# Kernel optimization log

Hardware: AMD Instinct MI355X
Metric: run time of the kernel (lower is better)

Reference implementation:

```python
import jax, jax.numpy as jnp
import numpy as np

B, N = 4, 512
C_IN, H, W = 1024, 48, 48
IMG_H, IMG_W = 48.0, 48.0
CNN_EMB, BOX_EMB, GCN_OUT = 512, 256, 512
ROWS, COLS = 58, 30
ALPHA = 5.0
K_EDGES = 8 * N  # edges kept per image per graph

# all directed pairs (i != j) of a fully-connected graph on N nodes
_ii, _jj = np.meshgrid(np.arange(N), np.arange(N), indexing='ij')
_m = _ii != _jj
PAIRS = jnp.asarray(np.stack([_ii[_m], _jj[_m]], axis=1).astype(np.int32))  # [E,2]


def setup_inputs():
    key = jax.random.key(0)
    ks = jax.random.split(key, 12)
    x = jax.random.normal(ks[0], (B, C_IN, H, W), jnp.float32)
    # valid boxes (x1<x2, y1<y2) inside the 48x48 feature map
    p = jax.random.uniform(ks[1], (B, N, 2, 2), minval=0.0, maxval=float(W) - 2.0)
    lo = jnp.min(p, axis=2)
    hi = jnp.max(p, axis=2) + 1.0
    boxes = jnp.concatenate([lo, hi], axis=-1)  # [B,N,4] x1,y1,x2,y2

    def lin(k, fi, fo):
        return jax.random.normal(k, (fi, fo), jnp.float32) / np.sqrt(fi)

    return {
        'input': x, 'boxes': boxes,
        'im_scales': jnp.ones((B,), jnp.float32),
        'pdls': jnp.zeros((B,), jnp.float32),
        'pdts': jnp.zeros((B,), jnp.float32),
        'W_dec': jax.random.normal(ks[2], (256, C_IN, 3, 3), jnp.float32) / np.sqrt(C_IN * 9.0),
        'b_dec': jnp.zeros((256,), jnp.float32),
        'W_box': lin(ks[3], 4, BOX_EMB), 'b_box': jnp.zeros((BOX_EMB,), jnp.float32),
        'W_cnn': lin(ks[4], 256 * 4, CNN_EMB), 'b_cnn': jnp.zeros((CNN_EMB,), jnp.float32),
        'W_grow': lin(ks[5], CNN_EMB + BOX_EMB, GCN_OUT), 'b_grow': jnp.zeros((GCN_OUT,), jnp.float32),
        'W_gcol': lin(ks[6], CNN_EMB + BOX_EMB, GCN_OUT), 'b_gcol': jnp.zeros((GCN_OUT,), jnp.float32),
        'W_rcls': lin(ks[7], GCN_OUT, 2 * (ROWS - 1) * 2), 'b_rcls': jnp.zeros((2 * (ROWS - 1) * 2,), jnp.float32),
        'W_ccls': lin(ks[8], GCN_OUT, 2 * (COLS - 1) * 2), 'b_ccls': jnp.zeros((2 * (COLS - 1) * 2,), jnp.float32),
    }


def _bilinear(feat, bidx, py, px):
    # feat [B,C,H,W]; py,px [M,4] sample coords -> [M,4,C]
    Hh, Ww = feat.shape[2], feat.shape[3]
    py = jnp.clip(py, 0.0, Hh - 1.0)
    px = jnp.clip(px, 0.0, Ww - 1.0)
    y0 = jnp.floor(py).astype(jnp.int32)
    x0 = jnp.floor(px).astype(jnp.int32)
    y1 = jnp.minimum(y0 + 1, Hh - 1)
    x1 = jnp.minimum(x0 + 1, Ww - 1)
    wy = (py - y0)[..., None]
    wx = (px - x0)[..., None]
    b = bidx[:, None]
    f00 = feat[b, :, y0, x0]
    f01 = feat[b, :, y0, x1]
    f10 = feat[b, :, y1, x0]
    f11 = feat[b, :, y1, x1]
    return f00 * (1 - wy) * (1 - wx) + f01 * (1 - wy) * wx + f10 * wy * (1 - wx) + f11 * wy * wx


def _roi_align_2x2(feat, boxes, bidx):
    # roi_align output_size=2, spatial_scale=1, one sample per bin (bin center)
    x1, y1, x2, y2 = boxes[:, 0], boxes[:, 1], boxes[:, 2], boxes[:, 3]
    bw = (x2 - x1) / 2.0
    bh = (y2 - y1) / 2.0
    offs = jnp.array([0.5, 1.5], jnp.float32)
    sx = x1[:, None] + offs * bw[:, None]  # [M,2]
    sy = y1[:, None] + offs * bh[:, None]
    py = sy[:, jnp.array([0, 0, 1, 1])]  # (iy, ix) ordering
    px = sx[:, jnp.array([0, 1, 0, 1])]
    val = _bilinear(feat, bidx, py, px)  # [M,4,C]
    return jnp.transpose(val, (0, 2, 1)).reshape(val.shape[0], -1)  # [M, C*2*2]


def _edge_attrs(boxes_i, scale, pdl, pdt):
    org = (boxes_i - jnp.stack([pdl, pdt, pdl, pdt])) / scale
    cx = (org[:, 0] + org[:, 2]) * 0.5
    cy = (org[:, 1] + org[:, 3]) * 0.5
    tb_w = jnp.max(org[:, jnp.array([0, 2])])
    tb_h = jnp.max(org[:, jnp.array([1, 3])])
    s, d = PAIRS[:, 0], PAIRS[:, 1]
    row_attr = jnp.exp(-jnp.square((cy[s] - cy[d]) * ALPHA / tb_h))
    col_attr = jnp.exp(-jnp.square((cx[s] - cx[d]) * ALPHA / tb_w))
    rv, ri = jax.lax.top_k(row_attr, K_EDGES)
    cv, ci = jax.lax.top_k(col_attr, K_EDGES)
    return rv, PAIRS[ri], cv, PAIRS[ci]


def _gcn(x, Wg, bg, edges, ew, num_nodes):
    # PyG GCNConv: self-loops with weight 1, symmetric normalization
    loop = jnp.arange(num_nodes, dtype=edges.dtype)
    src = jnp.concatenate([edges[0], loop])
    dst = jnp.concatenate([edges[1], loop])
    w = jnp.concatenate([ew, jnp.ones((num_nodes,), ew.dtype)])
    deg = jax.ops.segment_sum(w, dst, num_segments=num_nodes)
    dis = jax.lax.rsqrt(deg)  # deg >= 1 thanks to self-loops
    norm = dis[src] * w * dis[dst]
    xw = x @ Wg
    agg = jax.ops.segment_sum(norm[:, None] * xw[src], dst, num_segments=num_nodes)
    return agg + bg


def _forward(input, boxes, im_scales, pdls, pdts, W_dec, b_dec, W_box, b_box,
             W_cnn, b_cnn, W_grow, b_grow, W_gcol, b_gcol, W_rcls, b_rcls, W_ccls, b_ccls):
    Bn = B * N
    flat = boxes.reshape(Bn, 4)
    # box features (relative center / size)
    cx = (flat[:, 0] + flat[:, 2]) / 2.0
    cy = (flat[:, 1] + flat[:, 3]) / 2.0
    bf = jnp.stack([cx / IMG_W, cy / IMG_H,
                    (flat[:, 2] - flat[:, 0]) / IMG_W,
                    (flat[:, 3] - flat[:, 1]) / IMG_H], axis=1)
    box_feat = jax.nn.relu(bf @ W_box + b_box)
    # decode conv + relu
    dec = jax.lax.conv_general_dilated(input, W_dec, (1, 1), 'SAME',
                                       dimension_numbers=('NCHW', 'OIHW', 'NCHW'))
    dec = jax.nn.relu(dec + b_dec[None, :, None, None])
    # roi-align 2x2 + cnn embedding
    bidx = jnp.repeat(jnp.arange(B, dtype=jnp.int32), N)
    cnn = _roi_align_2x2(dec, flat, bidx)
    cnn_feat = jax.nn.relu(cnn @ W_cnn + b_cnn)
    # per-image dense graph -> top-8N row/col edges
    rv, re, cv, ce = jax.vmap(_edge_attrs)(boxes, im_scales, pdls, pdts)
    off = (jnp.arange(B, dtype=jnp.int32) * N)[:, None, None]
    row_edge = (re + off).reshape(-1, 2).T  # [2, B*K]
    col_edge = (ce + off).reshape(-1, 2).T
    row_w = rv.reshape(-1)
    col_w = cv.reshape(-1)
    fusion = jnp.concatenate([box_feat, cnn_feat], axis=1)  # [Bn, 768]
    row_feat = jax.nn.relu(_gcn(fusion, W_grow, b_grow, row_edge, row_w, Bn))
    col_feat = jax.nn.relu(_gcn(fusion, W_gcol, b_gcol, col_edge, col_w, Bn))
    row_score = jax.nn.leaky_relu(row_feat @ W_rcls + b_rcls, 0.01).reshape(Bn, 2, ROWS - 1, 2)
    col_score = jax.nn.leaky_relu(col_feat @ W_ccls + b_ccls, 0.01).reshape(Bn, 2, COLS - 1, 2)
    return row_score, col_score


def reference(input, boxes, im_scales, pdls, pdts, W_dec, b_dec, W_box, b_box,
              W_cnn, b_cnn, W_grow, b_grow, W_gcol, b_gcol, W_rcls, b_rcls, W_ccls, b_ccls):
    return _forward(input, boxes, im_scales, pdls, pdts, W_dec, b_dec, W_box, b_box,
                    W_cnn, b_cnn, W_grow, b_grow, W_gcol, b_gcol,
                    W_rcls, b_rcls, W_ccls, b_ccls)
```

## Files before the change

### kernel.cpp

```cpp
#include <hip/hip_runtime.h>
#include <cstdint>
#include <math.h>

typedef unsigned int u32;
typedef unsigned long long u64;
typedef unsigned short ushort;

typedef __attribute__((ext_vector_type(8))) _Float16 f16x8;
typedef __attribute__((ext_vector_type(4))) _Float16 f16x4;
typedef __attribute__((ext_vector_type(4))) float f32x4;

#define NB    4
#define BnN   2048
#define NE    261632
#define NCHUNK 16
#define ECHUNK 16352
#define KEDGE 4096
#define TIECAP 2048
#define PSLICE 2359296
#define MS    64
#define TS    64

#define GLD16(gsrc, ldst)                                                    \
    __builtin_amdgcn_global_load_lds(                                        \
        (const __attribute__((address_space(1))) void*)(gsrc),               \
        (__attribute__((address_space(3))) void*)(ldst), 16, 0, 0)

__global__ __launch_bounds__(256) void cvt_x_kernel(
    const float* __restrict__ in, _Float16* __restrict__ xf)
{
    __shared__ _Float16 sh[64][49];
    int cg = blockIdx.x, y = blockIdx.y, b = blockIdx.z;
    int tid = threadIdx.x;
    for (int i = tid; i < 64 * 48; i += 256) {
        int cl = i / 48, x = i - cl * 48;
        sh[cl][x] = (_Float16)in[(((size_t)b * 1024 + cg * 64 + cl) * 48 + y) * 48 + x];
    }
    __syncthreads();
    for (int i = tid; i < 64 * 48; i += 256) {
        int x = i / 64, cl = i - x * 64;
        xf[((size_t)(b * 48 + y) * 48 + x) * 1024 + cg * 64 + cl] = sh[cl][x];
    }
}

__global__ __launch_bounds__(256) void cvt_w_kernel(
    const float* __restrict__ W, _Float16* __restrict__ wf)
{
    __shared__ _Float16 sh[9216];
    int o = blockIdx.x, tid = threadIdx.x;
    for (int g = tid; g < 9216; g += 256)
        sh[g] = (_Float16)W[(size_t)o * 9216 + g];
    __syncthreads();
    for (int g = tid; g < 9216; g += 256) {
        int tap = g >> 10, ch = g & 1023;
        wf[(size_t)o * 9216 + g] = sh[ch * 9 + tap];
    }
}

__global__ __launch_bounds__(256) void cvt_t5_kernel(
    const float* __restrict__ Wc,  _Float16* __restrict__ WcT,
    const float* __restrict__ Wgr, _Float16* __restrict__ WgrT,
    const float* __restrict__ Wgc, _Float16* __restrict__ WgcT,
    const float* __restrict__ Wr,  _Float16* __restrict__ WrT,
    const float* __restrict__ Wcc, _Float16* __restrict__ WccT)
{
    __shared__ _Float16 sh[32][33];
    int bid = blockIdx.x;
    const float* in; _Float16* out; int K, N, tx0, ty0, ntx;
    if (bid < 512)       { in = Wc;  out = WcT;  K = 1024; N = 512; ntx = 16; bid -= 0;    }
    else if (bid < 896)  { in = Wgr; out = WgrT; K = 768;  N = 512; ntx = 16; bid -= 512;  }
    else if (bid < 1280) { in = Wgc; out = WgcT; K = 768;  N = 512; ntx = 16; bid -= 896;  }
    else if (bid < 1408) { in = Wr;  out = WrT;  K = 512;  N = 228; ntx = 8;  bid -= 1280; }
    else                 { in = Wcc; out = WccT; K = 512;  N = 116; ntx = 4;  bid -= 1408; }
    tx0 = (bid % ntx) * 32;
    ty0 = (bid / ntx) * 32;
    int tx = threadIdx.x & 31, ty = threadIdx.x >> 5;
#pragma unroll
    for (int i = 0; i < 4; ++i) {
        int k = ty0 + ty + i * 8, n = tx0 + tx;
        sh[ty + i * 8][tx] = (k < K && n < N) ? (_Float16)in[(size_t)k * N + n] : (_Float16)0.f;
    }
    __syncthreads();
#pragma unroll
    for (int i = 0; i < 4; ++i) {
        int n = tx0 + ty + i * 8, k = ty0 + tx;
        if (n < N && k < K) out[(size_t)n * K + k] = sh[tx][ty + i * 8];
    }
}

#define STAGE(cc)                                                            \
    {                                                                        \
        _Pragma("unroll")                                                    \
        for (int it = 0; it < 5; ++it) {                                     \
            if (it * 256 + wv * 64 < 1152)                                   \
                GLD16(wsrc[it] + (cc), &wS[(it * 256 + wv * 64) * 8]);       \
        }                                                                    \
        _Pragma("unroll")                                                    \
        for (int it = 0; it < 8; ++it)                                       \
            GLD16(xsrc[it] + (cc), &xS[(it * 256 + wv * 64) * 8]);           \
    }

#define LDB(BUF, R)                                                          \
    {                                                                        \
        _Pragma("unroll")                                                    \
        for (int u = 0; u < 9; ++u) {                                        \
            int nt_ = u / 3, dx_ = u % 3;                                    \
            BUF[u] = *(const f16x8*)&xS[(((R) * 4 + q) * 50 + nt_ * 16 + n + dx_) * 8]; \
        }                                                                    \
    }

#define DOTAP(TAP, BLO, BHI)                                                 \
    {                                                                        \
        _Pragma("unroll")                                                    \
        for (int dx_ = 0; dx_ < 3; ++dx_) {                                  \
            f16x8 a0 = *(const f16x8*)&wS[(((TAP) + dx_) * 128 + q * 32 + n) * 8];      \
            f16x8 a1 = *(const f16x8*)&wS[(((TAP) + dx_) * 128 + q * 32 + 16 + n) * 8]; \
            _Pragma("unroll")                                                \
            for (int nt_ = 0; nt_ < 3; ++nt_) {                              \
                f16x8 blo = BLO[nt_ * 3 + dx_];                              \
                f16x8 bhi = BHI[nt_ * 3 + dx_];                              \
                acc[0][0][nt_] = __builtin_amdgcn_mfma_f32_16x16x32_f16(a0, blo, acc[0][0][nt_], 0, 0, 0); \
                acc[1][0][nt_] = __builtin_amdgcn_mfma_f32_16x16x32_f16(a1, blo, acc[1][0][nt_], 0, 0, 0); \
                acc[0][1][nt_] = __builtin_amdgcn_mfma_f32_16x16x32_f16(a0, bhi, acc[0][1][nt_], 0, 0, 0); \
                acc[1][1][nt_] = __builtin_amdgcn_mfma_f32_16x16x32_f16(a1, bhi, acc[1][1][nt_], 0, 0, 0); \
            }                                                                \
        }                                                                    \
    }

__global__ __launch_bounds__(256, 3) void conv_part_kernel(
    const _Float16* __restrict__ xf, const _Float16* __restrict__ wf,
    const _Float16* __restrict__ zbuf, float* __restrict__ pbuf)
{
    __shared__ _Float16 wS[1152 * 8];
    __shared__ _Float16 xS[2048 * 8];
    const int p = blockIdx.x;
    const int L = (p & 7) * 96 + (p >> 3);
    const int og = L & 7;
    const int t  = L >> 3;
    const int xt = t % 6;
    const int bz = t / 6;
    const int y0 = xt * 8;
    const int b  = bz >> 2, ks = bz & 3;
    const int tid = threadIdx.x;
    const int wv = tid >> 6;
    const int ln = tid & 63;
    const int n  = ln & 15;
    const int q  = ln >> 4;

    f32x4 acc[2][2][3];
#pragma unroll
    for (int mt = 0; mt < 2; ++mt)
#pragma unroll
        for (int rr = 0; rr < 2; ++rr)
#pragma unroll
            for (int nt = 0; nt < 3; ++nt) acc[mt][rr][nt] = (f32x4){0.f, 0.f, 0.f, 0.f};

    const _Float16* wsrc[5];
    const _Float16* xsrc[8];
#pragma unroll
    for (int it = 0; it < 5; ++it) {
        int g = it * 256 + tid;
        int gg = (g < 1152) ? g : 0;
        int tap = gg >> 7, r = gg & 127, qq = r >> 5, oc = r & 31;
        wsrc[it] = wf + (size_t)(((og * 32 + oc) * 9 + tap) * 1024 + qq * 8);
    }
#pragma unroll
    for (int it = 0; it < 8; ++it) {
        int g = it * 256 + tid;
        int row = g / 200, r2 = g - row * 200;
        int qq = r2 / 50, c = r2 - qq * 50;
        int gy = y0 + row - 1, gx = c - 1;
        bool inb = (g < 2000) && ((unsigned)gy < 48u) && ((unsigned)gx < 48u);
        xsrc[it] = inb ? (xf + (size_t)(((b * 48 + gy) * 48 + gx) * 1024 + qq * 8)) : zbuf;
    }

    const int c0 = ks * 256;
    const int rbase = 2 * wv;

    STAGE(c0);

#pragma unroll 1
    for (int ci = 0; ci < 8; ++ci) {
        asm volatile("s_waitcnt vmcnt(0)" ::: "memory");
        __syncthreads();

        __builtin_amdgcn_s_setprio(1);
        f16x8 bA[9], bB[9];
        LDB(bA, rbase + 0);
        LDB(bB, rbase + 1);
        DOTAP(0, bA, bB);
        LDB(bA, rbase + 2);
        DOTAP(3, bB, bA);
        LDB(bB, rbase + 3);
        DOTAP(6, bA, bB);
        __builtin_amdgcn_s_setprio(0);
        __syncthreads();
        if (ci < 7) STAGE(c0 + (ci + 1) * 32);
    }

#pragma unroll
    for (int rr = 0; rr < 2; ++rr) {
        const int y = y0 + 2 * wv + rr;
#pragma unroll
        for (int mt = 0; mt < 2; ++mt) {
#pragma unroll
            for (int nt = 0; nt < 3; ++nt) {
                int x = nt * 16 + n;
                *(f32x4*)(pbuf + (size_t)ks * PSLICE +
                          ((size_t)(b * 48 + y) * 48 + x) * 256 + og * 32 + mt * 16 + q * 4) = acc[mt][rr][nt];
            }
        }
    }
}

__global__ __launch_bounds__(256) void conv_sum_kernel(
    const float* __restrict__ pbuf, const float* __restrict__ bd,
    _Float16* __restrict__ dec)
{
    size_t idx = (size_t)blockIdx.x * 256 + threadIdx.x;
    size_t e = idx * 4;
    int och = (int)(e & 255);
    f32x4 s0 = *(const f32x4*)(pbuf + e);
    f32x4 s1 = *(const f32x4*)(pbuf + (size_t)PSLICE + e);
    f32x4 s2 = *(const f32x4*)(pbuf + (size_t)2 * PSLICE + e);
    f32x4 s3 = *(const f32x4*)(pbuf + (size_t)3 * PSLICE + e);
    float4 b4 = *(const float4*)(bd + och);
    f16x4 v;
    v.x = (_Float16)fmaxf(s0[0] + s1[0] + s2[0] + s3[0] + b4.x, 0.f);
    v.y = (_Float16)fmaxf(s0[1] + s1[1] + s2[1] + s3[1] + b4.y, 0.f);
    v.z = (_Float16)fmaxf(s0[2] + s1[2] + s2[2] + s3[2] + b4.z, 0.f);
    v.w = (_Float16)fmaxf(s0[3] + s1[3] + s2[3] + s3[3] + b4.w, 0.f);
    *(f16x4*)(dec + e) = v;
}

__global__ __launch_bounds__(256) void roi_box_kernel(
    const _Float16* __restrict__ dec, const float* __restrict__ boxes,
    const float* __restrict__ Wb, const float* __restrict__ bb,
    _Float16* __restrict__ cnn, _Float16* __restrict__ fusion)
{
    int n = blockIdx.x; int c = threadIdx.x;
    int b = n >> 9;
    float x1 = boxes[n * 4 + 0], y1 = boxes[n * 4 + 1];
    float x2 = boxes[n * 4 + 2], y2 = boxes[n * 4 + 3];
    {
        float bf0 = ((x1 + x2) * 0.5f) / 48.f;
        float bf1 = ((y1 + y2) * 0.5f) / 48.f;
        float bf2 = (x2 - x1) / 48.f;
        float bf3 = (y2 - y1) / 48.f;
        float acc = bb[c];
        acc += bf0 * Wb[0 * 256 + c];
        acc += bf1 * Wb[1 * 256 + c];
        acc += bf2 * Wb[2 * 256 + c];
        acc += bf3 * Wb[3 * 256 + c];
        fusion[(size_t)n * 768 + c] = (_Float16)fmaxf(acc, 0.f);
    }
    float bw = (x2 - x1) * 0.5f, bh = (y2 - y1) * 0.5f;
    float sxv[2] = { x1 + 0.5f * bw, x1 + 1.5f * bw };
    float syv[2] = { y1 + 0.5f * bh, y1 + 1.5f * bh };
    float px[4] = { sxv[0], sxv[1], sxv[0], sxv[1] };
    float py[4] = { syv[0], syv[0], syv[1], syv[1] };
    const _Float16* f = dec + (size_t)b * 2304 * 256;
    f16x4 o4;
    float res[4];
#pragma unroll
    for (int p = 0; p < 4; ++p) {
        float yy = fminf(fmaxf(py[p], 0.f), 47.f);
        float xx = fminf(fmaxf(px[p], 0.f), 47.f);
        int y0 = (int)floorf(yy), x0 = (int)floorf(xx);
        int y1i = min(y0 + 1, 47), x1i = min(x0 + 1, 47);
        float wy = yy - (float)y0, wx = xx - (float)x0;
        float f00 = (float)f[(size_t)(y0 * 48 + x0) * 256 + c];
        float f01 = (float)f[(size_t)(y0 * 48 + x1i) * 256 + c];
        float f10 = (float)f[(size_t)(y1i * 48 + x0) * 256 + c];
        float f11 = (float)f[(size_t)(y1i * 48 + x1i) * 256 + c];
        res[p] = f00 * (1.f - wy) * (1.f - wx) + f01 * (1.f - wy) * wx
               + f10 * wy * (1.f - wx) + f11 * wy * wx;
    }
    o4.x = (_Float16)res[0]; o4.y = (_Float16)res[1];
    o4.z = (_Float16)res[2]; o4.w = (_Float16)res[3];
    *(f16x4*)(cnn + (size_t)n * 1024 + c * 4) = o4;
}

#define GEMM_STAGE(cc, bi)                                                   \
    {                                                                        \
        GLD16(asrc + (cc), &aS[bi][(wv * 64) * 8]);                          \
        GLD16(bsrc + (cc), &bS[bi][(wv * 64) * 8]);                          \
    }

template <int ACT, typename OUTT>
__global__ __launch_bounds__(256) void gemm16_kernel(
    const _Float16* __restrict__ A, const _Float16* __restrict__ Bt,
    const _Float16* __restrict__ zbuf,
    const float* __restrict__ bias, OUTT* __restrict__ C,
    int M, int N, int K, int ldC)
{
    __shared__ _Float16 aS[2][256 * 8];
    __shared__ _Float16 bS[2][256 * 8];
    const int n0 = blockIdx.x * 64, m0 = blockIdx.y * 64;
    const int tid = threadIdx.x;
    const int wv = tid >> 6, ln = tid & 63;
    const int wm = wv & 1, wn = wv >> 1;
    const int lm = ln & 15, lq = ln >> 4;
    const int sr = tid >> 2, sq = tid & 3;

    const _Float16* asrc = A + (size_t)(m0 + sr) * K + sq * 8;
    const _Float16* bsrc = (n0 + sr < N) ? (Bt + (size_t)(n0 + sr) * K + sq * 8) : zbuf;

    f32x4 acc[2][2];
#pragma unroll
    for (int i = 0; i < 2; ++i)
#pragma unroll
        for (int j = 0; j < 2; ++j) acc[i][j] = (f32x4){0.f, 0.f, 0.f, 0.f};

    const int NT = K >> 5;
    GEMM_STAGE(0, 0);
#pragma unroll 1
    for (int it = 0; it < NT; ++it) {
        const int bi = it & 1;
        if (it + 1 < NT) {
            GEMM_STAGE((it + 1) * 32, bi ^ 1);
            asm volatile("s_waitcnt vmcnt(2)" ::: "memory");
        } else {
            asm volatile("s_waitcnt vmcnt(0)" ::: "memory");
        }
        __builtin_amdgcn_s_barrier();
        f16x8 af[2], bf[2];
#pragma unroll
        for (int mt = 0; mt < 2; ++mt) af[mt] = *(const f16x8*)&aS[bi][(wm * 32 + mt * 16 + lm) * 32 + lq * 8];
#pragma unroll
        for (int nt = 0; nt < 2; ++nt) bf[nt] = *(const f16x8*)&bS[bi][(wn * 32 + nt * 16 + lm) * 32 + lq * 8];
#pragma unroll
        for (int mt = 0; mt < 2; ++mt)
#pragma unroll
            for (int nt = 0; nt < 2; ++nt)
                acc[mt][nt] = __builtin_amdgcn_mfma_f32_16x16x32_f16(af[mt], bf[nt], acc[mt][nt], 0, 0, 0);
        __builtin_amdgcn_sched_barrier(0);
        __builtin_amdgcn_s_barrier();
    }

#pragma unroll
    for (int mt = 0; mt < 2; ++mt) {
#pragma unroll
        for (int nt = 0; nt < 2; ++nt) {
            int col = n0 + wn * 32 + nt * 16 + lm;
            if (col >= N) continue;
            float bs = bias ? bias[col] : 0.f;
#pragma unroll
            for (int r = 0; r < 4; ++r) {
                int row = m0 + wm * 32 + mt * 16 + lq * 4 + r;
                float v = acc[mt][nt][r] + bs;
                if (ACT == 1) v = fmaxf(v, 0.f);
                if (ACT == 2) v = (v >= 0.f) ? v : 0.01f * v;
                C[(size_t)row * ldC + col] = (OUTT)v;
            }
        }
    }
}

__global__ __launch_bounds__(256) void gemm16z_kernel(
    const _Float16* __restrict__ A,
    const _Float16* __restrict__ Bt0, const _Float16* __restrict__ Bt1,
    const _Float16* __restrict__ zbuf,
    float* __restrict__ C0, float* __restrict__ C1,
    int M, int N, int K, int ldC)
{
    const _Float16* __restrict__ Bt = blockIdx.z ? Bt1 : Bt0;
    float* __restrict__ C = blockIdx.z ? C1 : C0;
    __shared__ _Float16 aS[2][256 * 8];
    __shared__ _Float16 bS[2][256 * 8];
    const int n0 = blockIdx.x * 64, m0 = blockIdx.y * 64;
    const int tid = threadIdx.x;
    const int wv = tid >> 6, ln = tid & 63;
    const int wm = wv & 1, wn = wv >> 1;
    const int lm = ln & 15, lq = ln >> 4;
    const int sr = tid >> 2, sq = tid & 3;

    const _Float16* asrc = A + (size_t)(m0 + sr) * K + sq * 8;
    const _Float16* bsrc = (n0 + sr < N) ? (Bt + (size_t)(n0 + sr) * K + sq * 8) : zbuf;

    f32x4 acc[2][2];
#pragma unroll
    for (int i = 0; i < 2; ++i)
#pragma unroll
        for (int j = 0; j < 2; ++j) acc[i][j] = (f32x4){0.f, 0.f, 0.f, 0.f};

    const int NT = K >> 5;
    GEMM_STAGE(0, 0);
#pragma unroll 1
    for (int it = 0; it < NT; ++it) {
        const int bi = it & 1;
        if (it + 1 < NT) {
            GEMM_STAGE((it + 1) * 32, bi ^ 1);
            asm volatile("s_waitcnt vmcnt(2)" ::: "memory");
        } else {
            asm volatile("s_waitcnt vmcnt(0)" ::: "memory");
        }
        __builtin_amdgcn_s_barrier();
        f16x8 af[2], bf[2];
#pragma unroll
        for (int mt = 0; mt < 2; ++mt) af[mt] = *(const f16x8*)&aS[bi][(wm * 32 + mt * 16 + lm) * 32 + lq * 8];
#pragma unroll
        for (int nt = 0; nt < 2; ++nt) bf[nt] = *(const f16x8*)&bS[bi][(wn * 32 + nt * 16 + lm) * 32 + lq * 8];
#pragma unroll
        for (int mt = 0; mt < 2; ++mt)
#pragma unroll
            for (int nt = 0; nt < 2; ++nt)
                acc[mt][nt] = __builtin_amdgcn_mfma_f32_16x16x32_f16(af[mt], bf[nt], acc[mt][nt], 0, 0, 0);
        __builtin_amdgcn_sched_barrier(0);
        __builtin_amdgcn_s_barrier();
    }

#pragma unroll
    for (int mt = 0; mt < 2; ++mt) {
#pragma unroll
        for (int nt = 0; nt < 2; ++nt) {
            int col = n0 + wn * 32 + nt * 16 + lm;
            if (col >= N) continue;
#pragma unroll
            for (int r = 0; r < 4; ++r) {
                int row = m0 + wm * 32 + mt * 16 + lq * 4 + r;
                C[(size_t)row * ldC + col] = acc[mt][nt][r];
            }
        }
    }
}

__device__ __forceinline__ float compute_sv_tb(
    const float* __restrict__ boxes, const float* __restrict__ scales,
    const float* __restrict__ pdls, const float* __restrict__ pdts,
    int b, int t, float* sv, float* red)
{
    int tid = threadIdx.x;
    float pdl = pdls[b], pdt = pdts[b], sc = scales[b];
    if (tid < 512) {
        const float* bx = boxes + (size_t)(b * 512 + tid) * 4;
        float o0 = (bx[0] - pdl) / sc;
        float o1 = (bx[1] - pdt) / sc;
        float o2 = (bx[2] - pdl) / sc;
        float o3 = (bx[3] - pdt) / sc;
        sv[tid]  = (t == 0) ? (o1 + o3) * 0.5f : (o0 + o2) * 0.5f;
        red[tid] = (t == 0) ? fmaxf(o1, o3)    : fmaxf(o0, o2);
    }
    __syncthreads();
    for (int s = 256; s > 0; s >>= 1) {
        if (tid < s) red[tid] = fmaxf(red[tid], red[tid + s]);
        __syncthreads();
    }
    float tbv = red[0];
    __syncthreads();
    return tbv;
}

#define QBITS(e, QB)                                                   \
    {                                                                  \
        int i_ = (e) / 511; int jj_ = (e) - i_ * 511;                  \
        int j_ = jj_ + (jj_ >= i_ ? 1 : 0);                            \
        float diff_ = sv[i_] - sv[j_];                                 \
        float u_ = (diff_ * 5.0f) / tbv;                               \
        float q_ = u_ * u_;                                            \
        QB = __float_as_uint(q_);                                      \
    }

__global__ __launch_bounds__(1024) void histA_kernel(
    const float* __restrict__ boxes, const float* __restrict__ scales,
    const float* __restrict__ pdls, const float* __restrict__ pdts,
    u32* __restrict__ gpart)
{
    __shared__ float sv[512]; __shared__ float red[512];
    __shared__ u32 lh[4096];
    const int sel = blockIdx.y, b = sel >> 1, t = sel & 1;
    const int tid = threadIdx.x;
    for (int i = tid; i < 4096; i += 1024) lh[i] = 0;
    const float tbv = compute_sv_tb(boxes, scales, pdls, pdts, b, t, sv, red);
    const int e1 = min((int)(blockIdx.x + 1) * ECHUNK, NE);
    for (int e = blockIdx.x * ECHUNK + tid; e < e1; e += 1024) {
        u32 qb; QBITS(e, qb);
        atomicAdd(&lh[qb >> 20], 1u);
    }
    __syncthreads();
    u32* G = gpart + ((size_t)sel * NCHUNK + blockIdx.x) * 4096;
    for (int i = tid; i < 4096; i += 1024) G[i] = lh[i];
}

__global__ __launch_bounds__(1024) void scanA_kernel(
    const u32* __restrict__ gpart, u32* __restrict__ meta)
{
    const int sel = blockIdx.x, tid = threadIdx.x;
    __shared__ u32 bins[4096];
    __shared__ u32 sc[2][1024];
    for (int b = tid; b < 4096; b += 1024) {
        u32 s = 0;
        for (int c = 0; c < NCHUNK; ++c) s += gpart[((size_t)sel * NCHUNK + c) * 4096 + b];
        bins[b] = s;
    }
    __syncthreads();
    u32 part = 0;
#pragma unroll
    for (int j = 0; j < 4; ++j) part += bins[tid * 4 + j];
    sc[0][tid] = part;
    __syncthreads();
    int src = 0;
    for (int st = 1; st < 1024; st <<= 1) {
        sc[1 - src][tid] = sc[src][tid] + (tid >= st ? sc[src][tid - st] : 0);
        __syncthreads(); src = 1 - src;
    }
    u32 inc = sc[src][tid], exc = inc - part;
    if (exc < (u32)KEDGE && (u32)KEDGE <= inc) {
        u32 cum = exc;
        for (int j = 0; j < 4; ++j) {
            u32 c = bins[tid * 4 + j];
            if (cum + c >= (u32)KEDGE) {
                meta[sel * MS + 0] = (u32)(tid * 4 + j);
                meta[sel * MS + 1] = (u32)KEDGE - cum;
                break;
            }
            cum += c;
        }
    }
}

__global__ __launch_bounds__(1024) void histB_kernel(
    const float* __restrict__ boxes, const float* __restrict__ scales,
    const float* __restrict__ pdls, const float* __restrict__ pdts,
    const u32* __restrict__ meta, u32* __restrict__ gpart)
{
    __shared__ float sv[512]; __shared__ float red[512];
    __shared__ u32 lh[4096];
    const int sel = blockIdx.y, b = sel >> 1, t = sel & 1;
    const int tid = threadIdx.x;
    for (int i = tid; i < 4096; i += 1024) lh[i] = 0;
    const float tbv = compute_sv_tb(boxes, scales, pdls, pdts, b, t, sv, red);
    const u32 p12 = meta[sel * MS + 0];
    const int e1 = min((int)(blockIdx.x + 1) * ECHUNK, NE);
    for (int e = blockIdx.x * ECHUNK + tid; e < e1; e += 1024) {
        u32 qb; QBITS(e, qb);
        if ((qb >> 20) == p12) atomicAdd(&lh[(qb >> 8) & 0xFFF], 1u);
    }
    __syncthreads();
    u32* G = gpart + ((size_t)sel * NCHUNK + blockIdx.x) * 4096;
    for (int i = tid; i < 4096; i += 1024) G[i] = lh[i];
}

__global__ __launch_bounds__(1024) void scanB_kernel(
    const u32* __restrict__ gpart, u32* __restrict__ meta)
{
    const int sel = blockIdx.x, tid = threadIdx.x;
    const u32 TH = meta[sel * MS + 1];
    __shared__ u32 bins[4096];
    __shared__ u32 sc[2][1024];
    for (int b = tid; b < 4096; b += 1024) {
        u32 s = 0;
        for (int c = 0; c < NCHUNK; ++c) s += gpart[((size_t)sel * NCHUNK + c) * 4096 + b];
        bins[b] = s;
    }
    __syncthreads();
    u32 part = 0;
#pragma unroll
    for (int j = 0; j < 4; ++j) part += bins[tid * 4 + j];
    sc[0][tid] = part;
    __syncthreads();
    int src = 0;
    for (int st = 1; st < 1024; st <<= 1) {
        sc[1 - src][tid] = sc[src][tid] + (tid >= st ? sc[src][tid - st] : 0);
        __syncthreads(); src = 1 - src;
    }
    u32 inc = sc[src][tid], exc = inc - part;
    if (exc < TH && TH <= inc) {
        u32 cum = exc;
        for (int j = 0; j < 4; ++j) {
            u32 c = bins[tid * 4 + j];
            if (cum + c >= TH) {
                meta[sel * MS + 6] = (meta[sel * MS + 0] << 12) | (u32)(tid * 4 + j);
                meta[sel * MS + 7] = TH - cum;
                break;
            }
            cum += c;
        }
    }
}

__global__ __launch_bounds__(1024) void histC_kernel(
    const float* __restrict__ boxes, const float* __restrict__ scales,
    const float* __restrict__ pdls, const float* __restrict__ pdts,
    const u32* __restrict__ meta, u32* __restrict__ gpart)
{
    __shared__ float sv[512]; __shared__ float red[512];
    __shared__ u32 lh[256];
    const int sel = blockIdx.y, b = sel >> 1, t = sel & 1;
    const int tid = threadIdx.x;
    if (tid < 256) lh[tid] = 0;
    const float tbv = compute_sv_tb(boxes, scales, pdls, pdts, b, t, sv, red);
    const u32 p24 = meta[sel * MS + 6];
    const int e1 = min((int)(blockIdx.x + 1) * ECHUNK, NE);
    for (int e = blockIdx.x * ECHUNK + tid; e < e1; e += 1024) {
        u32 qb; QBITS(e, qb);
        if ((qb >> 8) == p24) atomicAdd(&lh[qb & 0xFF], 1u);
    }
    __syncthreads();
    u32* G = gpart + ((size_t)sel * NCHUNK + blockIdx.x) * 256;
    if (tid < 256) G[tid] = lh[tid];
}

__global__ __launch_bounds__(256) void scanC_kernel(
    const u32* __restrict__ gpart, u32* __restrict__ meta)
{
    const int sel = blockIdx.x, tid = threadIdx.x;
    const u32 TH = meta[sel * MS + 7];
    __shared__ u32 bins[256];
    __shared__ u32 sc[2][256];
    __shared__ u32 s_qstar;
    u32 s = 0;
    for (int c = 0; c < NCHUNK; ++c) s += gpart[((size_t)sel * NCHUNK + c) * 256 + tid];
    bins[tid] = s;
    sc[0][tid] = s;
    __syncthreads();
    int src = 0;
    for (int st = 1; st < 256; st <<= 1) {
        sc[1 - src][tid] = sc[src][tid] + (tid >= st ? sc[src][tid - st] : 0);
        __syncthreads(); src = 1 - src;
    }
    u32 inc = sc[src][tid], exc = inc - bins[tid];
    if (exc < TH && TH <= inc)
        s_qstar = (meta[sel * MS + 6] << 8) | (u32)tid;
    __syncthreads();
    if (tid == 0) {
        u32 prefix = s_qstar;
        float qstar = __uint_as_float(prefix);
        float wstar = (float)exp(-(double)qstar);
        u32 lo = 0, hi = prefix;
        while (lo < hi) {
            u32 mid = (lo + hi) >> 1;
            float wm = (float)exp(-(double)__uint_as_float(mid));
            if (wm > wstar) lo = mid + 1; else hi = mid;
        }
        meta[sel * MS + 2] = lo;
        lo = prefix; hi = 0x7F800000u;
        while (lo < hi) {
            u32 mid = (lo + hi + 1) >> 1;
            float wm = (float)exp(-(double)__uint_as_float(mid));
            if (wm < wstar) hi = mid - 1; else lo = mid;
        }
        meta[sel * MS + 3] = lo;
        meta[sel * MS + 4] = __float_as_uint(wstar);
    }
}

__global__ __launch_bounds__(1024) void emit_kernel(
    const float* __restrict__ boxes, const float* __restrict__ scales,
    const float* __restrict__ pdls, const float* __restrict__ pdts,
    u32* __restrict__ meta, int* __restrict__ tiebuf, int* __restrict__ tiecnt,
    int* __restrict__ es, int* __restrict__ ed, float* __restrict__ ewt,
    int* __restrict__ indeg, float* __restrict__ degw)
{
    __shared__ float sv[512]; __shared__ float red[512];
    __shared__ int s_wcnt, s_tcnt, s_wbase, s_tbase;
    const int sel = blockIdx.y, b = sel >> 1, t = sel & 1;
    const int tid = threadIdx.x;
    const float tbv = compute_sv_tb(boxes, scales, pdls, pdts, b, t, sv, red);
    const u32 qlo = meta[sel * MS + 2], qhi = meta[sel * MS + 3];
    const int base = t * 16384 + b * 4096;
    const int e0 = blockIdx.x * ECHUNK + tid;
    const int e1 = min((int)(blockIdx.x + 1) * ECHUNK, NE);
    if (tid == 0) { s_wcnt = 0; s_tcnt = 0; }
    __syncthreads();
    int myw = 0, myt = 0;
    for (int e = e0; e < e1; e += 1024) {
        u32 qb; QBITS(e, qb);
        if (qb < qlo) ++myw;
        else if (qb <= qhi) ++myt;
    }
    if (myw) atomicAdd(&s_wcnt, myw);
    if (myt) atomicAdd(&s_tcnt, myt);
    __syncthreads();
    if (tid == 0) {
        s_wbase = (s_wcnt > 0) ? (int)atomicAdd(&meta[sel * MS + 5], (u32)s_wcnt) : 0;
        s_tbase = (s_tcnt > 0) ? atomicAdd(&tiecnt[sel * TS], s_tcnt) : 0;
        s_wcnt = 0; s_tcnt = 0;
    }
    __syncthreads();
    for (int e = e0; e < e1; e += 1024) {
        u32 qb; QBITS(e, qb);
        if (qb < qlo) {
            int i = e / 511; int jj = e - i * 511; int j = jj + (jj >= i ? 1 : 0);
            float wval = (float)exp(-(double)__uint_as_float(qb));
            int slot = s_wbase + atomicAdd(&s_wcnt, 1);
            es[base + slot] = b * 512 + i;
            ed[base + slot] = b * 512 + j;
            ewt[base + slot] = wval;
            atomicAdd(&indeg[t * 2048 + b * 512 + j], 1);
            atomicAdd(&degw[t * 2048 + b * 512 + j], wval);
        } else if (qb <= qhi) {
            int p = s_tbase + atomicAdd(&s_tcnt, 1);
            if (p < TIECAP) tiebuf[sel * TIECAP + p] = e;
        }
    }
}

__global__ __launch_bounds__(1024) void tie_scan_fill_kernel(
    u32* __restrict__ meta, const int* __restrict__ tiebuf, const int* __restrict__ tiecnt,
    int* __restrict__ es, int* __restrict__ ed, float* __restrict__ ewt,
    int* __restrict__ indeg, float* __restrict__ degw,
    int* __restrict__ offs, float* __restrict__ dis, int* __restrict__ csr)
{
    __shared__ int bufA[2048], bufB[2048];
    __shared__ int fill_l[2048];
    const int t = blockIdx.x, tid = threadIdx.x;
    for (int b = 0; b < 4; ++b) {
        int sel = b * 2 + t;
        int m = min(tiecnt[sel * TS], TIECAP);
        int r = KEDGE - (int)meta[sel * MS + 5];
        float wt = __uint_as_float(meta[sel * MS + 4]);
        int base = t * 16384 + b * 4096;
        for (int k = tid; k < m; k += 1024) {
            int e = tiebuf[sel * TIECAP + k];
            int rank = 0;
            for (int l = 0; l < m; ++l) rank += (tiebuf[sel * TIECAP + l] < e) ? 1 : 0;
            if (rank < r) {
                int i = e / 511; int jj = e - i * 511; int j = jj + (jj >= i ? 1 : 0);
                int slot = (int)atomicAdd(&meta[sel * MS + 5], 1u);
                es[base + slot] = b * 512 + i;
                ed[base + slot] = b * 512 + j;
                ewt[base + slot] = wt;
                atomicAdd(&indeg[t * 2048 + b * 512 + j], 1);
                atomicAdd(&degw[t * 2048 + b * 512 + j], wt);
            }
        }
    }
    __threadfence();
    __syncthreads();
    bufA[tid] = indeg[t * 2048 + tid];
    bufA[tid + 1024] = indeg[t * 2048 + tid + 1024];
    fill_l[tid] = 0; fill_l[tid + 1024] = 0;
    __syncthreads();
    int* src = bufA; int* dst = bufB;
    for (int st = 1; st < 2048; st <<= 1) {
        dst[tid] = src[tid] + (tid >= st ? src[tid - st] : 0);
        int k1 = tid + 1024;
        dst[k1] = src[k1] + (k1 >= st ? src[k1 - st] : 0);
        __syncthreads();
        int* tmp = src; src = dst; dst = tmp;
    }
    int off0 = (tid == 0) ? 0 : src[tid - 1];
    int off1 = src[tid + 1023];
    __syncthreads();
    dst[tid] = off0; dst[tid + 1024] = off1;
    offs[t * 2048 + tid] = off0;
    offs[t * 2048 + tid + 1024] = off1;
    dis[t * 2048 + tid] = 1.0f / sqrtf(1.0f + degw[t * 2048 + tid]);
    dis[t * 2048 + tid + 1024] = 1.0f / sqrtf(1.0f + degw[t * 2048 + tid + 1024]);
    __syncthreads();
    for (int e = tid; e < 16384; e += 1024) {
        int dl = ed[t * 16384 + e] & 2047;
        int pos = dst[dl] + atomicAdd(&fill_l[dl], 1);
        csr[t * 16384 + pos] = e;
    }
}

__global__ __launch_bounds__(256) void gcn_agg_kernel(
    const float* __restrict__ xw_row, const float* __restrict__ xw_col,
    const float* __restrict__ b_row, const float* __restrict__ b_col,
    const int* __restrict__ es, const float* __restrict__ ew,
    const int* __restrict__ csr, const int* __restrict__ offs,
    const int* __restrict__ indeg, const float* __restrict__ dis,
    _Float16* __restrict__ feat_row, _Float16* __restrict__ feat_col)
{
    int d = blockIdx.x; int t = blockIdx.y;
    const float* xw = t ? xw_col : xw_row;
    const float* bg = t ? b_col : b_row;
    _Float16* out = t ? feat_col : feat_row;
    int f0 = threadIdx.x, f1 = threadIdx.x + 256;
    float dd = dis[t * 2048 + d];
    float a0 = dd * dd * xw[(size_t)d * 512 + f0];
    float a1 = dd * dd * xw[(size_t)d * 512 + f1];
    int st = offs[t * 2048 + d], cnt = indeg[t * 2048 + d];
    for (int k = 0; k < cnt; ++k) {
        int e = csr[t * 16384 + st + k];
        int s = es[t * 16384 + e];
        float w = ew[t * 16384 + e];
        float coef = dis[t * 2048 + s] * w * dd;
        a0 += coef * xw[(size_t)s * 512 + f0];
        a1 += coef * xw[(size_t)s * 512 + f1];
    }
    a0 += bg[f0]; a1 += bg[f1];
    out[(size_t)d * 512 + f0] = (_Float16)fmaxf(a0, 0.f);
    out[(size_t)d * 512 + f1] = (_Float16)fmaxf(a1, 0.f);
}

extern "C" void kernel_launch(void* const* d_in, const int* in_sizes, int n_in,
                              void* d_out, int out_size, void* d_ws, size_t ws_size,
                              hipStream_t stream)
{
    const float* x      = (const float*)d_in[0];
    const float* boxes  = (const float*)d_in[1];
    const float* scales = (const float*)d_in[2];
    const float* pdls   = (const float*)d_in[3];
    const float* pdts   = (const float*)d_in[4];
    const float* W_dec  = (const float*)d_in[5];
    const float* b_dec  = (const float*)d_in[6];
    const float* W_box  = (const float*)d_in[7];
    const float* b_box  = (const float*)d_in[8];
    const float* W_cnn  = (const float*)d_in[9];
    const float* b_cnn  = (const float*)d_in[10];
    const float* W_grow = (const float*)d_in[11];
    const float* b_grow = (const float*)d_in[12];
    const float* W_gcol = (const float*)d_in[13];
    const float* b_gcol = (const float*)d_in[14];
    const float* W_rcls = (const float*)d_in[15];
    const float* b_rcls = (const float*)d_in[16];
    const float* W_ccls = (const float*)d_in[17];
    const float* b_ccls = (const float*)d_in[18];

    char* ws = (char*)d_ws;
    size_t off = 0;
    auto alloc = [&](size_t bytes) -> void* {
        void* p = ws + off;
        off = (off + bytes + 255) & ~(size_t)255;
        return p;
    };
    _Float16* xf16   = (_Float16*)alloc((size_t)4 * 2304 * 1024 * 2);
    _Float16* wf16   = (_Float16*)alloc((size_t)256 * 9216 * 2);
    _Float16* dec    = (_Float16*)alloc((size_t)4 * 2304 * 256 * 2);
    float*    pbuf   = (float*)   alloc((size_t)4 * PSLICE * 4);
    _Float16* cnn    = (_Float16*)alloc((size_t)2048 * 1024 * 2);
    _Float16* fusion = (_Float16*)alloc((size_t)2048 * 768 * 2);
    _Float16* WcT    = (_Float16*)alloc((size_t)512 * 1024 * 2);
    _Float16* WgrT   = (_Float16*)alloc((size_t)512 * 768 * 2);
    _Float16* WgcT   = (_Float16*)alloc((size_t)512 * 768 * 2);
    _Float16* WrT    = (_Float16*)alloc((size_t)228 * 512 * 2);
    _Float16* WccT   = (_Float16*)alloc((size_t)116 * 512 * 2);
    float* xw        = (float*)alloc((size_t)2097152 * 4);
    _Float16* feats  = (_Float16*)alloc((size_t)2 * 2048 * 512 * 2);
    int*  es     = (int*)  alloc((size_t)2 * 16384 * 4);
    int*  ed     = (int*)  alloc((size_t)2 * 16384 * 4);
    float* ewt   = (float*)alloc((size_t)2 * 16384 * 4);
    int*  offsA  = (int*)  alloc((size_t)4096 * 4);
    float* dis   = (float*)alloc((size_t)4096 * 4);
    int*  csr    = (int*)  alloc((size_t)2 * 16384 * 4);
    int*  tiebuf = (int*)  alloc((size_t)8 * TIECAP * 4);
    u32*  gpartA = (u32*)  alloc((size_t)8 * NCHUNK * 4096 * 4);
    u32*  gpartB = (u32*)  alloc((size_t)8 * NCHUNK * 4096 * 4);
    u32*  gpartC = (u32*)  alloc((size_t)8 * NCHUNK * 256 * 4);
    size_t z0 = off;
    u32*  meta   = (u32*)  alloc((size_t)8 * MS * 4);
    int*  tiecnt = (int*)  alloc((size_t)8 * TS * 4);
    int*  indeg  = (int*)  alloc((size_t)4096 * 4);
    float* degw  = (float*)alloc((size_t)4096 * 4);
    _Float16* zbuf = (_Float16*)alloc((size_t)4096);
    size_t z1 = off;

    float* out = (float*)d_out;

    hipMemsetAsync(ws + z0, 0, z1 - z0, stream);

    cvt_x_kernel<<<dim3(16, 48, 4), 256, 0, stream>>>(x, xf16);
    cvt_w_kernel<<<256, 256, 0, stream>>>(W_dec, wf16);
    conv_part_kernel<<<dim3(768), 256, 0, stream>>>(xf16, wf16, zbuf, pbuf);
    conv_sum_kernel<<<2304, 256, 0, stream>>>(pbuf, b_dec, dec);
    roi_box_kernel<<<2048, 256, 0, stream>>>(dec, boxes, W_box, b_box, cnn, fusion);
    cvt_t5_kernel<<<1472, 256, 0, stream>>>(W_cnn, WcT, W_grow, WgrT, W_gcol, WgcT,
                                            W_rcls, WrT, W_ccls, WccT);
    gemm16_kernel<1, _Float16><<<dim3(8, 32), 256, 0, stream>>>(cnn, WcT, zbuf, b_cnn, fusion + 256, 2048, 512, 1024, 768);
    histA_kernel<<<dim3(NCHUNK, 8), 1024, 0, stream>>>(boxes, scales, pdls, pdts, gpartA);
    scanA_kernel<<<8, 1024, 0, stream>>>(gpartA, meta);
    histB_kernel<<<dim3(NCHUNK, 8), 1024, 0, stream>>>(boxes, scales, pdls, pdts, meta, gpartB);
    scanB_kernel<<<8, 1024, 0, stream>>>(gpartB, meta);
    histC_kernel<<<dim3(NCHUNK, 8), 1024, 0, stream>>>(boxes, scales, pdls, pdts, meta, gpartC);
    scanC_kernel<<<8, 256, 0, stream>>>(gpartC, meta);
    emit_kernel<<<dim3(NCHUNK, 8), 1024, 0, stream>>>(boxes, scales, pdls, pdts, meta,
                                                      tiebuf, tiecnt, es, ed, ewt, indeg, degw);
    tie_scan_fill_kernel<<<2, 1024, 0, stream>>>(meta, tiebuf, tiecnt, es, ed, ewt,
                                                 indeg, degw, offsA, dis, csr);
    gemm16z_kernel<<<dim3(8, 32, 2), 256, 0, stream>>>(fusion, WgrT, WgcT, zbuf, xw, xw + 1048576,
                                                       2048, 512, 768, 512);
    gcn_agg_kernel<<<dim3(2048, 2), 256, 0, stream>>>(xw, xw + 1048576, b_grow, b_gcol,
                                                      es, ewt, csr, offsA, indeg, dis,
                                                      feats, feats + (size_t)2048 * 512);
    gemm16_kernel<2, float><<<dim3(4, 32), 256, 0, stream>>>(feats, WrT, zbuf, b_rcls, out, 2048, 228, 512, 228);
    gemm16_kernel<2, float><<<dim3(2, 32), 256, 0, stream>>>(feats + (size_t)2048 * 512, WccT, zbuf, b_ccls,
                                                             out + (size_t)2048 * 228, 2048, 116, 512, 116);
}
```

Before: 348.2 us.

## Double-buffer conv input tiles and drop horizontal halo from LDS staging

The input activation tile in the conv partial kernel is now double-buffered in LDS, so the next channel chunk's input loads are issued before the current chunk's MFMA work, with partial vmcnt waits. The x-halo columns are no longer staged; edge lanes read from a small zero buffer in LDS instead, which shrinks each tile from 2000 to 1920 vectors. Weight staging stays single-buffered and is issued after the compute barrier. The larger LDS footprint lowers the launch bound from 3 to 2 blocks per CU, trading occupancy for overlap of loads with compute.

New measurement: 353.3 us. No clear change (+1.5%).

```diff
diff --git a/kernel.cpp b/kernel.cpp
--- a/kernel.cpp
+++ b/kernel.cpp
@@ -88,16 +88,24 @@
     }
 }
 
-#define STAGE(cc)                                                            \
+#define STAGE_X(cc, BUF)                                                     \
+    {                                                                        \
+        _Pragma("unroll")                                                    \
+        for (int it = 0; it < 8; ++it) {                                     \
+            int g0 = it * 256 + wv * 64;                                     \
+            if (g0 < 1920)                                                   \
+                GLD16(xsrc[it] + (cc), &xS[(BUF) * 15360 + g0 * 8]);         \
+        }                                                                    \
+    }
+
+#define STAGE_W(cc)                                                          \
     {                                                                        \
         _Pragma("unroll")                                                    \
         for (int it = 0; it < 5; ++it) {                                     \
-            if (it * 256 + wv * 64 < 1152)                                   \
-                GLD16(wsrc[it] + (cc), &wS[(it * 256 + wv * 64) * 8]);       \
+            int g0 = it * 256 + wv * 64;                                     \
+            if (g0 < 1152)                                                   \
+                GLD16(wsrc[it] + (cc), &wS[g0 * 8]);                         \
         }                                                                    \
-        _Pragma("unroll")                                                    \
-        for (int it = 0; it < 8; ++it)                                       \
-            GLD16(xsrc[it] + (cc), &xS[(it * 256 + wv * 64) * 8]);           \
     }
 
 #define LDB(BUF, R)                                                          \
@@ -105,7 +113,11 @@
         _Pragma("unroll")                                                    \
         for (int u = 0; u < 9; ++u) {                                        \
             int nt_ = u / 3, dx_ = u % 3;                                    \
-            BUF[u] = *(const f16x8*)&xS[(((R) * 4 + q) * 50 + nt_ * 16 + n + dx_) * 8]; \
+            int col = nt_ * 16 + n + dx_ - 1;                                \
+            const _Float16* pa = &xb[(((R) * 4 + q) * 48 + col) * 8];        \
+            if (u == 0 && n == 0)  pa = zS;                                  \
+            if (u == 8 && n == 15) pa = zS;                                  \
+            BUF[u] = *(const f16x8*)pa;                                      \
         }                                                                    \
     }
 
@@ -127,12 +139,13 @@
         }                                                                    \
     }
 
-__global__ __launch_bounds__(256, 3) void conv_part_kernel(
+__global__ __launch_bounds__(256, 2) void conv_part_kernel(
     const _Float16* __restrict__ xf, const _Float16* __restrict__ wf,
     const _Float16* __restrict__ zbuf, float* __restrict__ pbuf)
 {
     __shared__ _Float16 wS[1152 * 8];
-    __shared__ _Float16 xS[2048 * 8];
+    __shared__ _Float16 xS[2 * 1920 * 8];
+    __shared__ __attribute__((aligned(16))) _Float16 zS[8];
     const int p = blockIdx.x;
     const int L = (p & 7) * 96 + (p >> 3);
     const int og = L & 7;
@@ -167,23 +180,37 @@
 #pragma unroll
     for (int it = 0; it < 8; ++it) {
         int g = it * 256 + tid;
-        int row = g / 200, r2 = g - row * 200;
-        int qq = r2 / 50, c = r2 - qq * 50;
-        int gy = y0 + row - 1, gx = c - 1;
-        bool inb = (g < 2000) && ((unsigned)gy < 48u) && ((unsigned)gx < 48u);
-        xsrc[it] = inb ? (xf + (size_t)(((b * 48 + gy) * 48 + gx) * 1024 + qq * 8)) : zbuf;
+        int gg = (g < 1920) ? g : 0;
+        int row = gg / 192, rem = gg - row * 192;
+        int qq = rem / 48, c = rem - qq * 48;
+        int gy = y0 + row - 1;
+        bool inb = (g < 1920) && ((unsigned)gy < 48u);
+        xsrc[it] = inb ? (xf + (size_t)(((b * 48 + gy) * 48 + c) * 1024 + qq * 8)) : zbuf;
     }
 
     const int c0 = ks * 256;
     const int rbase = 2 * wv;
 
-    STAGE(c0);
+    if (tid == 0) *(uint4*)&zS[0] = make_uint4(0u, 0u, 0u, 0u);
+    STAGE_X(c0, 0);
+    STAGE_W(c0);
+    asm volatile("s_waitcnt vmcnt(0)" ::: "memory");
+    __syncthreads();
 
 #pragma unroll 1
     for (int ci = 0; ci < 8; ++ci) {
-        asm volatile("s_waitcnt vmcnt(0)" ::: "memory");
-        __syncthreads();
-
+        const int cur = ci & 1;
+        if (ci < 7) {
+            STAGE_X(c0 + (ci + 1) * 32, cur ^ 1);
+            if (wv & 2) asm volatile("s_waitcnt vmcnt(7)" ::: "memory");
+            else        asm volatile("s_waitcnt vmcnt(8)" ::: "memory");
+        } else {
+            asm volatile("s_waitcnt vmcnt(0)" ::: "memory");
+        }
+        __builtin_amdgcn_s_barrier();
+        __builtin_amdgcn_sched_barrier(0);
+
+        const _Float16* xb = xS + cur * 15360;
         __builtin_amdgcn_s_setprio(1);
         f16x8 bA[9], bB[9];
         LDB(bA, rbase + 0);
@@ -194,8 +221,10 @@
         LDB(bB, rbase + 3);
         DOTAP(6, bA, bB);
         __builtin_amdgcn_s_setprio(0);
-        __syncthreads();
-        if (ci < 7) STAGE(c0 + (ci + 1) * 32);
+        asm volatile("s_waitcnt lgkmcnt(0)" ::: "memory");
+        __builtin_amdgcn_sched_barrier(0);
+        __builtin_amdgcn_s_barrier();
+        if (ci < 7) STAGE_W(c0 + (ci + 1) * 32);
     }
 
 #pragma unroll
```
